# Kernel optimization log

Hardware: AMD Instinct MI355X
Metric: run time of the kernel (lower is better)

Reference implementation:

```python
import jax, jax.numpy as jnp
import numpy as np

N_TX, N_CARD, N_MERCH = 200000, 50000, 10000
E = 200000
TX_IN, EMB, H = 128, 64, 128
N_LAYERS, N_ETYPES = 2, 4  # etypes: 0 card->tx, 1 tx->card, 2 merch->tx, 3 tx->merch


def setup_inputs() -> dict:
    key = jax.random.key(0)
    ks = jax.random.split(key, 24)
    s = 0.05
    inp = {
        "tx_x": jax.random.normal(ks[0], (N_TX, TX_IN), jnp.float32),
        "card_ids": jnp.arange(N_CARD, dtype=jnp.int64),
        "merch_ids": jnp.arange(N_MERCH, dtype=jnp.int64),
        "e_card": jax.random.randint(ks[1], (E,), 0, N_CARD),
        "e_tx_c": jnp.arange(E, dtype=jnp.int64),
        "e_merch": jax.random.randint(ks[2], (E,), 0, N_MERCH),
        "e_tx_m": jnp.arange(E, dtype=jnp.int64),
        # parameters
        "card_emb": jax.random.normal(ks[3], (N_CARD, EMB), jnp.float32) * s,
        "merch_emb": jax.random.normal(ks[4], (N_MERCH, EMB), jnp.float32) * s,
        "card_proj_W": jax.random.normal(ks[5], (EMB, H), jnp.float32) * s,
        "card_proj_b": jnp.zeros((H,), jnp.float32),
        "merch_proj_W": jax.random.normal(ks[6], (EMB, H), jnp.float32) * s,
        "merch_proj_b": jnp.zeros((H,), jnp.float32),
        "tx_W": jax.random.normal(ks[7], (TX_IN, H), jnp.float32) * s,
        "tx_b": jnp.zeros((H,), jnp.float32),
        "conv_Wl": jax.random.normal(ks[8], (N_LAYERS, N_ETYPES, H, H), jnp.float32) * s,
        "conv_bl": jnp.zeros((N_LAYERS, N_ETYPES, H), jnp.float32),
        "conv_Wr": jax.random.normal(ks[9], (N_LAYERS, N_ETYPES, H, H), jnp.float32) * s,
        "h1_W": jax.random.normal(ks[10], (H, H), jnp.float32) * s,
        "h1_b": jnp.zeros((H,), jnp.float32),
        "h2_W": jax.random.normal(ks[11], (H, 1), jnp.float32) * s,
        "h2_b": jnp.zeros((1,), jnp.float32),
    }
    return inp


def _sage(x_src, x_dst, src, dst, Wl, bl, Wr, n_dst):
    # PyG SAGEConv: mean-aggregate neighbor features, then lin_l(agg)+lin_r(x_dst)
    agg = jax.ops.segment_sum(x_src[src], dst, num_segments=n_dst)
    cnt = jax.ops.segment_sum(jnp.ones((src.shape[0],), x_src.dtype), dst, num_segments=n_dst)
    mean = agg / jnp.maximum(cnt, 1.0)[:, None]
    return mean @ Wl + bl + x_dst @ Wr


def reference(tx_x, card_ids, merch_ids, e_card, e_tx_c, e_merch, e_tx_m,
              card_emb, merch_emb, card_proj_W, card_proj_b, merch_proj_W, merch_proj_b,
              tx_W, tx_b, conv_Wl, conv_bl, conv_Wr, h1_W, h1_b, h2_W, h2_b):
    # input encoders (dropout inactive at eval)
    h_tx = jax.nn.relu(tx_x @ tx_W + tx_b)
    h_card = card_emb[card_ids] @ card_proj_W + card_proj_b
    h_merch = merch_emb[merch_ids] @ merch_proj_W + merch_proj_b

    for l in range(N_LAYERS):
        Wl, bl, Wr = conv_Wl[l], conv_bl[l], conv_Wr[l]
        # HeteroConv aggr='sum' across edge types sharing a dst type
        o_tx = (_sage(h_card, h_tx, e_card, e_tx_c, Wl[0], bl[0], Wr[0], N_TX)
                + _sage(h_merch, h_tx, e_merch, e_tx_m, Wl[2], bl[2], Wr[2], N_TX))
        o_card = _sage(h_tx, h_card, e_tx_c, e_card, Wl[1], bl[1], Wr[1], N_CARD)
        o_merch = _sage(h_tx, h_merch, e_tx_m, e_merch, Wl[3], bl[3], Wr[3], N_MERCH)
        h_tx, h_card, h_merch = jax.nn.relu(o_tx), jax.nn.relu(o_card), jax.nn.relu(o_merch)

    logits = (jax.nn.relu(h_tx @ h1_W + h1_b) @ h2_W + h2_b).reshape(-1)
    return logits
```

## Files before the change

kernel.cpp:

```cpp
#include <hip/hip_runtime.h>


#define N_TX    200000
#define N_CARD  50000
#define N_MERCH 10000
#define NE      200000

typedef __attribute__((ext_vector_type(8))) short short8;
typedef __attribute__((ext_vector_type(4))) float f32x4;

__device__ inline unsigned short f2b(float f) {
    unsigned u = __builtin_bit_cast(unsigned, f);
    unsigned r = (u + 0x7fffu + ((u >> 16) & 1u)) >> 16;
    return (unsigned short)r;
}
__device__ inline float b2f(unsigned short s) {
    return __builtin_bit_cast(float, (unsigned)s << 16);
}

__global__ __launch_bounds__(256, 3) void fused2(
    const void* __restrict__ A, int a_f32,
    const unsigned short* __restrict__ W1T, const float* __restrict__ b1,
    const unsigned short* __restrict__ W2T, const float* __restrict__ b2,
    const unsigned short* __restrict__ P1, const int* __restrict__ I1,
    const unsigned short* __restrict__ P2, const int* __restrict__ I2,
    unsigned short* __restrict__ OUT0,
    const float* __restrict__ h2w, const float* __restrict__ h2b,
    void* __restrict__ OUT1, int M)
{
    __shared__ float Tf[64 * 132];
    __shared__ unsigned short Tb[64 * 136];
    const int tid  = threadIdx.x;
    const int wave = tid >> 6;
    const int lane = tid & 63;
    const int quad = lane >> 4;
    const int l15  = lane & 15;
    const int base = blockIdx.x * 64;
    const int rgrp = tid >> 4;
    const int c0   = l15 * 8;
    const bool modeA = (OUT0 != nullptr);

    int idx1[4], idx2[4];
#pragma unroll
    for (int p = 0; p < 4; ++p) {
        int r = base + p * 16 + rgrp;
        int rc = (r < M) ? r : 0;
        idx1[p] = I1 ? I1[rc] : 0;
        idx2[p] = I2 ? I2[rc] : 0;
    }

    short8 af[4];
    {
        int r = base + wave * 16 + l15;
        int rc = (r < M) ? r : 0;
        if (a_f32) {
            const float* ap = (const float*)A + (size_t)rc * 128 + quad * 8;
#pragma unroll
            for (int kk = 0; kk < 4; ++kk) {
                float4 u = *reinterpret_cast<const float4*>(ap + kk * 32);
                float4 v = *reinterpret_cast<const float4*>(ap + kk * 32 + 4);
                short8 t;
                t[0] = (short)f2b(u.x); t[1] = (short)f2b(u.y);
                t[2] = (short)f2b(u.z); t[3] = (short)f2b(u.w);
                t[4] = (short)f2b(v.x); t[5] = (short)f2b(v.y);
                t[6] = (short)f2b(v.z); t[7] = (short)f2b(v.w);
                af[kk] = t;
            }
        } else {
            const unsigned short* ap =
                (const unsigned short*)A + (size_t)rc * 128 + quad * 8;
#pragma unroll
            for (int kk = 0; kk < 4; ++kk)
                af[kk] = *reinterpret_cast<const short8*>(ap + kk * 32);
        }
    }

    f32x4 acc[8];
#pragma unroll
    for (int nt = 0; nt < 8; ++nt) acc[nt] = (f32x4){0.f, 0.f, 0.f, 0.f};
#pragma unroll
    for (int nt = 0; nt < 8; ++nt) {
        const unsigned short* bp = W1T + (nt * 16 + l15) * 128 + quad * 8;
#pragma unroll
        for (int kk = 0; kk < 4; ++kk) {
            short8 bf = *reinterpret_cast<const short8*>(bp + kk * 32);
            acc[nt] = __builtin_amdgcn_mfma_f32_16x16x32_bf16(
                af[kk], bf, acc[nt], 0, 0, 0);
        }
    }

    short8 p1v[4], p2v[4];
    if (P1) {
#pragma unroll
        for (int p = 0; p < 4; ++p)
            p1v[p] = *reinterpret_cast<const short8*>(
                P1 + (size_t)idx1[p] * 128 + c0);
    }
    if (P2) {
#pragma unroll
        for (int p = 0; p < 4; ++p)
            p2v[p] = *reinterpret_cast<const short8*>(
                P2 + (size_t)idx2[p] * 128 + c0);
    }

    const int lrow0 = wave * 16 + quad * 4;
    if (modeA) {
#pragma unroll
        for (int nt = 0; nt < 8; ++nt) {
            float bb = b1 ? b1[nt * 16 + l15] : 0.f;
#pragma unroll
            for (int reg = 0; reg < 4; ++reg)
                Tb[(lrow0 + reg) * 136 + nt * 16 + l15] =
                    f2b(fmaxf(acc[nt][reg] + bb, 0.f));
        }
    } else {
#pragma unroll
        for (int nt = 0; nt < 8; ++nt)
#pragma unroll
            for (int reg = 0; reg < 4; ++reg)
                Tf[(lrow0 + reg) * 132 + nt * 16 + l15] = acc[nt][reg];
    }
    __syncthreads();

    if (modeA) {
#pragma unroll
        for (int p = 0; p < 4; ++p) {
            const int rloc = p * 16 + rgrp;
            const int r = base + rloc;
            if (r < M) {
                short8 hv = *reinterpret_cast<const short8*>(&Tb[rloc * 136 + c0]);
                *reinterpret_cast<short8*>(OUT0 + (size_t)r * 128 + c0) = hv;
            }
        }
    } else {
        float b1r[8];
#pragma unroll
        for (int j = 0; j < 8; ++j) b1r[j] = b1 ? b1[c0 + j] : 0.f;
#pragma unroll
        for (int p = 0; p < 4; ++p) {
            const int rloc = p * 16 + rgrp;
            float4 u = *reinterpret_cast<const float4*>(&Tf[rloc * 132 + c0]);
            float4 v = *reinterpret_cast<const float4*>(&Tf[rloc * 132 + c0 + 4]);
            float o[8] = {u.x, u.y, u.z, u.w, v.x, v.y, v.z, v.w};
            short8 ov;
#pragma unroll
            for (int j = 0; j < 8; ++j) {
                float t = o[j] + b1r[j];
                if (P1) t += b2f((unsigned short)p1v[p][j]);
                if (P2) t += b2f((unsigned short)p2v[p][j]);
                ov[j] = (short)f2b(fmaxf(t, 0.f));
            }
            *reinterpret_cast<short8*>(&Tb[rloc * 136 + c0]) = ov;
        }
        __syncthreads();
    }

    short8 af2[4];
#pragma unroll
    for (int kk = 0; kk < 4; ++kk)
        af2[kk] = *reinterpret_cast<const short8*>(
            &Tb[(wave * 16 + l15) * 136 + quad * 8 + kk * 32]);

    f32x4 acc2[8];
#pragma unroll
    for (int nt = 0; nt < 8; ++nt) acc2[nt] = (f32x4){0.f, 0.f, 0.f, 0.f};
#pragma unroll
    for (int nt = 0; nt < 8; ++nt) {
        const unsigned short* bp = W2T + (nt * 16 + l15) * 128 + quad * 8;
#pragma unroll
        for (int kk = 0; kk < 4; ++kk) {
            short8 bf = *reinterpret_cast<const short8*>(bp + kk * 32);
            acc2[nt] = __builtin_amdgcn_mfma_f32_16x16x32_bf16(
                af2[kk], bf, acc2[nt], 0, 0, 0);
        }
    }

    if (!modeA) {
        float hsum[4] = {0.f, 0.f, 0.f, 0.f};
#pragma unroll
        for (int nt = 0; nt < 8; ++nt) {
            float bb = b2 ? b2[nt * 16 + l15] : 0.f;
            float w = h2w[nt * 16 + l15];
#pragma unroll
            for (int reg = 0; reg < 4; ++reg) {
                float o = fmaxf(acc2[nt][reg] + bb, 0.f);
                hsum[reg] += o * w;
            }
        }
        float* OUTf = (float*)OUT1;
#pragma unroll
        for (int reg = 0; reg < 4; ++reg) {
            float h = hsum[reg];
            h += __shfl_xor(h, 1);
            h += __shfl_xor(h, 2);
            h += __shfl_xor(h, 4);
            h += __shfl_xor(h, 8);
            int r = base + wave * 16 + quad * 4 + reg;
            if (l15 == 0 && r < M) OUTf[r] = h + h2b[0];
        }
    } else {
#pragma unroll
        for (int nt = 0; nt < 8; ++nt)
#pragma unroll
            for (int reg = 0; reg < 4; ++reg)
                Tf[(lrow0 + reg) * 132 + nt * 16 + l15] = acc2[nt][reg];
        __syncthreads();
        float b2r[8];
#pragma unroll
        for (int j = 0; j < 8; ++j) b2r[j] = b2 ? b2[c0 + j] : 0.f;
        unsigned short* OB = (unsigned short*)OUT1;
#pragma unroll
        for (int p = 0; p < 4; ++p) {
            const int rloc = p * 16 + rgrp;
            const int r = base + rloc;
            float4 u = *reinterpret_cast<const float4*>(&Tf[rloc * 132 + c0]);
            float4 v = *reinterpret_cast<const float4*>(&Tf[rloc * 132 + c0 + 4]);
            float o[8] = {u.x, u.y, u.z, u.w, v.x, v.y, v.z, v.w};
            short8 ov;
#pragma unroll
            for (int j = 0; j < 8; ++j) {
                float t = o[j] + b2r[j];
                if (P1) t += b2f((unsigned short)p1v[p][j]);
                if (P2) t += b2f((unsigned short)p2v[p][j]);
                ov[j] = (short)f2b(fmaxf(t, 0.f));
            }
            if (r < M)
                *reinterpret_cast<short8*>(OB + (size_t)r * 128 + c0) = ov;
        }
    }
}

__global__ __launch_bounds__(256, 3) void fusedE_both(
    const float* __restrict__ Ac, const unsigned short* __restrict__ W1Tc,
    const float* __restrict__ b1c, const unsigned short* __restrict__ W2Tc,
    unsigned short* __restrict__ OUT0c, unsigned short* __restrict__ OUT1c,
    int Mc, int nbc,
    const float* __restrict__ Am, const unsigned short* __restrict__ W1Tm,
    const float* __restrict__ b1m, const unsigned short* __restrict__ W2Tm,
    unsigned short* __restrict__ OUT0m, unsigned short* __restrict__ OUT1m,
    int Mm)
{
    __shared__ float Tf[64 * 132];
    __shared__ unsigned short Tb[64 * 136];
    const bool isC = (int)blockIdx.x < nbc;
    const int bx   = isC ? blockIdx.x : blockIdx.x - nbc;
    const float* A = isC ? Ac : Am;
    const unsigned short* W1T = isC ? W1Tc : W1Tm;
    const float* b1 = isC ? b1c : b1m;
    const unsigned short* W2T = isC ? W2Tc : W2Tm;
    unsigned short* OUT0 = isC ? OUT0c : OUT0m;
    unsigned short* OUT1 = isC ? OUT1c : OUT1m;
    const int M = isC ? Mc : Mm;

    const int tid  = threadIdx.x;
    const int wave = tid >> 6;
    const int lane = tid & 63;
    const int quad = lane >> 4;
    const int l15  = lane & 15;
    const int base = bx * 64;
    const int rgrp = tid >> 4;
    const int c0   = l15 * 8;

    short8 af[2];
    {
        int r = base + wave * 16 + l15;
        int rc = (r < M) ? r : 0;
        const float* ap = A + (size_t)rc * 64 + quad * 8;
#pragma unroll
        for (int kk = 0; kk < 2; ++kk) {
            float4 u = *reinterpret_cast<const float4*>(ap + kk * 32);
            float4 v = *reinterpret_cast<const float4*>(ap + kk * 32 + 4);
            short8 t;
            t[0] = (short)f2b(u.x); t[1] = (short)f2b(u.y);
            t[2] = (short)f2b(u.z); t[3] = (short)f2b(u.w);
            t[4] = (short)f2b(v.x); t[5] = (short)f2b(v.y);
            t[6] = (short)f2b(v.z); t[7] = (short)f2b(v.w);
            af[kk] = t;
        }
    }

    f32x4 acc[8];
#pragma unroll
    for (int nt = 0; nt < 8; ++nt) acc[nt] = (f32x4){0.f, 0.f, 0.f, 0.f};
#pragma unroll
    for (int nt = 0; nt < 8; ++nt) {
        const unsigned short* bp = W1T + (nt * 16 + l15) * 64 + quad * 8;
#pragma unroll
        for (int kk = 0; kk < 2; ++kk) {
            short8 bf = *reinterpret_cast<const short8*>(bp + kk * 32);
            acc[nt] = __builtin_amdgcn_mfma_f32_16x16x32_bf16(
                af[kk], bf, acc[nt], 0, 0, 0);
        }
    }

    const int lrow0 = wave * 16 + quad * 4;
#pragma unroll
    for (int nt = 0; nt < 8; ++nt) {
        float bb = b1 ? b1[nt * 16 + l15] : 0.f;
#pragma unroll
        for (int reg = 0; reg < 4; ++reg)
            Tb[(lrow0 + reg) * 136 + nt * 16 + l15] = f2b(acc[nt][reg] + bb);
    }
    __syncthreads();

#pragma unroll
    for (int p = 0; p < 4; ++p) {
        const int rloc = p * 16 + rgrp;
        const int r = base + rloc;
        if (r < M) {
            short8 hv = *reinterpret_cast<const short8*>(&Tb[rloc * 136 + c0]);
            *reinterpret_cast<short8*>(OUT0 + (size_t)r * 128 + c0) = hv;
        }
    }

    short8 af2[4];
#pragma unroll
    for (int kk = 0; kk < 4; ++kk)
        af2[kk] = *reinterpret_cast<const short8*>(
            &Tb[(wave * 16 + l15) * 136 + quad * 8 + kk * 32]);

    f32x4 acc2[8];
#pragma unroll
    for (int nt = 0; nt < 8; ++nt) acc2[nt] = (f32x4){0.f, 0.f, 0.f, 0.f};
#pragma unroll
    for (int nt = 0; nt < 8; ++nt) {
        const unsigned short* bp = W2T + (nt * 16 + l15) * 128 + quad * 8;
#pragma unroll
        for (int kk = 0; kk < 4; ++kk) {
            short8 bf = *reinterpret_cast<const short8*>(bp + kk * 32);
            acc2[nt] = __builtin_amdgcn_mfma_f32_16x16x32_bf16(
                af2[kk], bf, acc2[nt], 0, 0, 0);
        }
    }
#pragma unroll
    for (int nt = 0; nt < 8; ++nt)
#pragma unroll
        for (int reg = 0; reg < 4; ++reg)
            Tf[(lrow0 + reg) * 132 + nt * 16 + l15] = acc2[nt][reg];
    __syncthreads();
#pragma unroll
    for (int p = 0; p < 4; ++p) {
        const int rloc = p * 16 + rgrp;
        const int r = base + rloc;
        if (r >= M) continue;
        float4 u = *reinterpret_cast<const float4*>(&Tf[rloc * 132 + c0]);
        float4 v = *reinterpret_cast<const float4*>(&Tf[rloc * 132 + c0 + 4]);
        float o[8] = {u.x, u.y, u.z, u.w, v.x, v.y, v.z, v.w};
        short8 ov;
#pragma unroll
        for (int j = 0; j < 8; ++j) ov[j] = (short)f2b(o[j]);
        *reinterpret_cast<short8*>(OUT1 + (size_t)r * 128 + c0) = ov;
    }
}

__global__ __launch_bounds__(256, 3) void fusedU2_both(
    const unsigned short* __restrict__ h_src,
    const int* __restrict__ offs_c, const int* __restrict__ eidx_c,
    const unsigned short* __restrict__ A2c,
    const unsigned short* __restrict__ W1aTc, const unsigned short* __restrict__ W1bTc,
    const float* __restrict__ b1c, const unsigned short* __restrict__ W2Tc,
    unsigned short* __restrict__ OUTc, int Mc, int nbc,
    const int* __restrict__ offs_m, const int* __restrict__ eidx_m,
    const unsigned short* __restrict__ A2m,
    const unsigned short* __restrict__ W1aTm, const unsigned short* __restrict__ W1bTm,
    const float* __restrict__ b1m, const unsigned short* __restrict__ W2Tm,
    unsigned short* __restrict__ OUTm, int Mm)
{
    __shared__ float Tf[64 * 132];
    __shared__ unsigned short Tb[64 * 136];
    const bool isC = (int)blockIdx.x < nbc;
    const int bx   = isC ? blockIdx.x : blockIdx.x - nbc;
    const int* offs = isC ? offs_c : offs_m;
    const int* eidx = isC ? eidx_c : eidx_m;
    const unsigned short* A2 = isC ? A2c : A2m;
    const unsigned short* W1aT = isC ? W1aTc : W1aTm;
    const unsigned short* W1bT = isC ? W1bTc : W1bTm;
    const float* b1 = isC ? b1c : b1m;
    const unsigned short* W2T = isC ? W2Tc : W2Tm;
    unsigned short* OUT1 = isC ? OUTc : OUTm;
    const int M = isC ? Mc : Mm;

    const int tid  = threadIdx.x;
    const int wave = tid >> 6;
    const int lane = tid & 63;
    const int quad = lane >> 4;
    const int l15  = lane & 15;
    const int base = bx * 64;
    const int rgrp = tid >> 4;
    const int c0   = l15 * 8;

    for (int n = 0; n < 16; ++n) {
        const int d = base + wave * 16 + n;
        int s = 0, e = 0;
        if (d < M) { s = offs[d]; e = offs[d + 1]; }
        float a[8] = {0.f, 0.f, 0.f, 0.f, 0.f, 0.f, 0.f, 0.f};
        for (int p = s + quad; p < e; p += 4) {
            int tx = eidx[p];
            short8 v = *reinterpret_cast<const short8*>(
                h_src + (size_t)tx * 128 + l15 * 8);
#pragma unroll
            for (int j = 0; j < 8; ++j) a[j] += b2f((unsigned short)v[j]);
        }
#pragma unroll
        for (int j = 0; j < 8; ++j) {
            a[j] += __shfl_xor(a[j], 16);
            a[j] += __shfl_xor(a[j], 32);
        }
        if (quad == 0 && d < M) {
            const float inv = (e > s) ? 1.0f / (float)(e - s) : 0.f;
            short8 o;
#pragma unroll
            for (int j = 0; j < 8; ++j) o[j] = (short)f2b(a[j] * inv);
            *reinterpret_cast<short8*>(&Tb[(wave * 16 + n) * 136 + l15 * 8]) = o;
        }
    }
    __syncthreads();

    short8 afa[4], afb[4];
    {
        int r = base + wave * 16 + l15;
        int rc = (r < M) ? r : 0;
        const unsigned short* a2 = A2 + (size_t)rc * 128 + quad * 8;
#pragma unroll
        for (int kk = 0; kk < 4; ++kk) {
            afa[kk] = *reinterpret_cast<const short8*>(
                &Tb[(wave * 16 + l15) * 136 + quad * 8 + kk * 32]);
            afb[kk] = *reinterpret_cast<const short8*>(a2 + kk * 32);
        }
    }

    f32x4 acc[8];
#pragma unroll
    for (int nt = 0; nt < 8; ++nt) acc[nt] = (f32x4){0.f, 0.f, 0.f, 0.f};
#pragma unroll
    for (int nt = 0; nt < 8; ++nt) {
        const unsigned short* bpa = W1aT + (nt * 16 + l15) * 128 + quad * 8;
        const unsigned short* bpb = W1bT + (nt * 16 + l15) * 128 + quad * 8;
#pragma unroll
        for (int kk = 0; kk < 4; ++kk) {
            short8 ba = *reinterpret_cast<const short8*>(bpa + kk * 32);
            acc[nt] = __builtin_amdgcn_mfma_f32_16x16x32_bf16(
                afa[kk], ba, acc[nt], 0, 0, 0);
            short8 bb = *reinterpret_cast<const short8*>(bpb + kk * 32);
            acc[nt] = __builtin_amdgcn_mfma_f32_16x16x32_bf16(
                afb[kk], bb, acc[nt], 0, 0, 0);
        }
    }
    __syncthreads();

    const int lrow0 = wave * 16 + quad * 4;
#pragma unroll
    for (int nt = 0; nt < 8; ++nt) {
        float bv = b1 ? b1[nt * 16 + l15] : 0.f;
#pragma unroll
        for (int reg = 0; reg < 4; ++reg)
            Tb[(lrow0 + reg) * 136 + nt * 16 + l15] =
                f2b(fmaxf(acc[nt][reg] + bv, 0.f));
    }
    __syncthreads();

    short8 af2[4];
#pragma unroll
    for (int kk = 0; kk < 4; ++kk)
        af2[kk] = *reinterpret_cast<const short8*>(
            &Tb[(wave * 16 + l15) * 136 + quad * 8 + kk * 32]);

    f32x4 acc2[8];
#pragma unroll
    for (int nt = 0; nt < 8; ++nt) acc2[nt] = (f32x4){0.f, 0.f, 0.f, 0.f};
#pragma unroll
    for (int nt = 0; nt < 8; ++nt) {
        const unsigned short* bp = W2T + (nt * 16 + l15) * 128 + quad * 8;
#pragma unroll
        for (int kk = 0; kk < 4; ++kk) {
            short8 bf = *reinterpret_cast<const short8*>(bp + kk * 32);
            acc2[nt] = __builtin_amdgcn_mfma_f32_16x16x32_bf16(
                af2[kk], bf, acc2[nt], 0, 0, 0);
        }
    }
#pragma unroll
    for (int nt = 0; nt < 8; ++nt)
#pragma unroll
        for (int reg = 0; reg < 4; ++reg)
            Tf[(lrow0 + reg) * 132 + nt * 16 + l15] = acc2[nt][reg];
    __syncthreads();
#pragma unroll
    for (int p = 0; p < 4; ++p) {
        const int rloc = p * 16 + rgrp;
        const int r = base + rloc;
        if (r >= M) continue;
        float4 u = *reinterpret_cast<const float4*>(&Tf[rloc * 132 + c0]);
        float4 v = *reinterpret_cast<const float4*>(&Tf[rloc * 132 + c0 + 4]);
        float o[8] = {u.x, u.y, u.z, u.w, v.x, v.y, v.z, v.w};
        short8 ov;
#pragma unroll
        for (int j = 0; j < 8; ++j) ov[j] = (short)f2b(o[j]);
        *reinterpret_cast<short8*>(OUT1 + (size_t)r * 128 + c0) = ov;
    }
}

__global__ __launch_bounds__(256) void convert_weights(
    const float* __restrict__ tx_W, const float* __restrict__ card_proj_W,
    const float* __restrict__ merch_proj_W, const float* __restrict__ h1_W,
    const float* __restrict__ conv_Wl, const float* __restrict__ conv_Wr,
    const float* __restrict__ conv_bl,
    unsigned short* __restrict__ WT, float* __restrict__ bsum)
{
    int job = blockIdx.y;
    int K = 128;
    const float* src = nullptr;
    const float* src2 = nullptr;
    if (job == 0) src = tx_W;
    else if (job == 1) { src = card_proj_W; K = 64; }
    else if (job == 2) { src = merch_proj_W; K = 64; }
    else if (job == 3) src = h1_W;
    else {
        int l = (job - 4) / 7, e = (job - 4) % 7;
        const float* Wl = conv_Wl + (size_t)l * 4 * 16384;
        const float* Wr = conv_Wr + (size_t)l * 4 * 16384;
        switch (e) {
            case 0: src = Wl; break;
            case 1: src = Wl + 16384; break;
            case 2: src = Wl + 2 * 16384; break;
            case 3: src = Wl + 3 * 16384; break;
            case 4: src = Wr + 16384; break;
            case 5: src = Wr + 3 * 16384; break;
            default:
                src = Wr; src2 = Wr + 2 * 16384;
                if (blockIdx.x == 0 && threadIdx.x < 128) {
                    const float* bl = conv_bl + (size_t)l * 4 * 128;
                    bsum[l * 128 + threadIdx.x] =
                        bl[threadIdx.x] + bl[2 * 128 + threadIdx.x];
                }
                break;
        }
    }
    int e = blockIdx.x * 256 + threadIdx.x;
    if (e < (K << 7)) {
        int n = (K == 128) ? (e >> 7) : (e >> 6);
        int k = e & (K - 1);
        float v = src[(size_t)k * 128 + n];
        if (src2) v += src2[(size_t)k * 128 + n];
        WT[(size_t)job * 16384 + n * K + k] = f2b(v);
    }
}

__global__ __launch_bounds__(256) void hist_kernel(
    const int* __restrict__ e_card, const int* __restrict__ e_merch,
    int* __restrict__ hist_c, int* __restrict__ hist_m, int E)
{
    int i = blockIdx.x * 256 + threadIdx.x;
    if (i < E) {
        atomicAdd(&hist_c[e_card[i]], 1);
        atomicAdd(&hist_m[e_merch[i]], 1);
    }
}

__global__ __launch_bounds__(1024) void scan2_kernel(
    const int* __restrict__ hist_c, int* __restrict__ offs_c, int* __restrict__ cur_c, int nc,
    const int* __restrict__ hist_m, int* __restrict__ offs_m, int* __restrict__ cur_m, int nm)
{
    const int* hist = (blockIdx.x == 0) ? hist_c : hist_m;
    int* offs = (blockIdx.x == 0) ? offs_c : offs_m;
    int* cursor = (blockIdx.x == 0) ? cur_c : cur_m;
    int n = (blockIdx.x == 0) ? nc : nm;
    __shared__ int wsum[16];
    __shared__ int s_carry;
    const int tid = threadIdx.x, lane = tid & 63, wid = tid >> 6;
    if (tid == 0) s_carry = 0;
    __syncthreads();
    for (int base = 0; base < n; base += 8192) {
        const int i0 = base + tid * 8;
        int v[8];
        int tot = 0;
#pragma unroll
        for (int j = 0; j < 8; ++j) {
            int idx = i0 + j;
            v[j] = (idx < n) ? hist[idx] : 0;
            tot += v[j];
        }
        int x = tot;
#pragma unroll
        for (int d = 1; d < 64; d <<= 1) {
            int t = __shfl_up(x, d);
            if (lane >= d) x += t;
        }
        if (lane == 63) wsum[wid] = x;
        __syncthreads();
        if (wid == 0) {
            int y = (lane < 16) ? wsum[lane] : 0;
#pragma unroll
            for (int d = 1; d < 16; d <<= 1) {
                int t = __shfl_up(y, d);
                if (lane >= d) y += t;
            }
            if (lane < 16) wsum[lane] = y;
        }
        __syncthreads();
        int wbase = (wid > 0) ? wsum[wid - 1] : 0;
        int run = s_carry + wbase + x - tot;
#pragma unroll
        for (int j = 0; j < 8; ++j) {
            int idx = i0 + j;
            if (idx < n) { offs[idx] = run; cursor[idx] = run; }
            run += v[j];
        }
        __syncthreads();
        if (tid == 0) s_carry += wsum[15];
        __syncthreads();
    }
    if (threadIdx.x == 0) offs[n] = s_carry;
}

__global__ __launch_bounds__(256) void place_kernel(
    const int* __restrict__ e_card, const int* __restrict__ e_tx_c,
    const int* __restrict__ e_merch, const int* __restrict__ e_tx_m,
    int* __restrict__ cur_c, int* __restrict__ eidx_c,
    int* __restrict__ cur_m, int* __restrict__ eidx_m, int E)
{
    int i = blockIdx.x * 256 + threadIdx.x;
    if (i < E) {
        int pc = atomicAdd(&cur_c[e_card[i]], 1);
        eidx_c[pc] = e_tx_c[i];
        int pm = atomicAdd(&cur_m[e_merch[i]], 1);
        eidx_m[pm] = e_tx_m[i];
    }
}

extern "C" void kernel_launch(void* const* d_in, const int* in_sizes, int n_in,
                              void* d_out, int out_size, void* d_ws, size_t ws_size,
                              hipStream_t stream)
{
    const float* tx_x        = (const float*)d_in[0];
    const int*   e_card      = (const int*)d_in[3];
    const int*   e_tx_c      = (const int*)d_in[4];
    const int*   e_merch     = (const int*)d_in[5];
    const int*   e_tx_m      = (const int*)d_in[6];
    const float* card_emb    = (const float*)d_in[7];
    const float* merch_emb   = (const float*)d_in[8];
    const float* card_proj_W = (const float*)d_in[9];
    const float* card_proj_b = (const float*)d_in[10];
    const float* merch_proj_W= (const float*)d_in[11];
    const float* merch_proj_b= (const float*)d_in[12];
    const float* tx_W        = (const float*)d_in[13];
    const float* tx_b        = (const float*)d_in[14];
    const float* conv_Wl     = (const float*)d_in[15];
    const float* conv_bl     = (const float*)d_in[16];
    const float* conv_Wr     = (const float*)d_in[17];
    const float* h1_W        = (const float*)d_in[18];
    const float* h1_b        = (const float*)d_in[19];
    const float* h2_W        = (const float*)d_in[20];
    const float* h2_b        = (const float*)d_in[21];

    char* wsb = (char*)d_ws;
    auto alloc = [&](size_t bytes) {
        char* p = wsb; wsb += (bytes + 255) & ~(size_t)255; return p;
    };
    unsigned short* h_tx0    = (unsigned short*)alloc((size_t)N_TX * 128 * 2);
    unsigned short* h_tx1    = (unsigned short*)alloc((size_t)N_TX * 128 * 2);
    unsigned short* h_card0  = (unsigned short*)alloc((size_t)N_CARD * 128 * 2);
    unsigned short* h_merch0 = (unsigned short*)alloc((size_t)N_MERCH * 128 * 2);
    unsigned short* p_card   = (unsigned short*)alloc((size_t)N_CARD * 128 * 2);
    unsigned short* p_merch  = (unsigned short*)alloc((size_t)N_MERCH * 128 * 2);
    unsigned short* WT       = (unsigned short*)alloc((size_t)18 * 16384 * 2);
    float* bsum = (float*)alloc(2 * 128 * 4);
    int* hist_c = (int*)alloc((size_t)(N_CARD + N_MERCH) * 4);
    int* hist_m = hist_c + N_CARD;
    int* offs_c = (int*)alloc((size_t)(N_CARD + 1) * 4);
    int* cur_c  = (int*)alloc((size_t)N_CARD * 4);
    int* eidx_c = (int*)alloc((size_t)NE * 4);
    int* offs_m = (int*)alloc((size_t)(N_MERCH + 1) * 4);
    int* cur_m  = (int*)alloc((size_t)N_MERCH * 4);
    int* eidx_m = (int*)alloc((size_t)NE * 4);

    auto WTj = [&](int job) { return WT + (size_t)job * 16384; };

    const int nbc = (N_CARD + 63) / 64;
    const int nbm = (N_MERCH + 63) / 64;

    convert_weights<<<dim3(64, 18), dim3(256), 0, stream>>>(
        tx_W, card_proj_W, merch_proj_W, h1_W, conv_Wl, conv_Wr, conv_bl,
        WT, bsum);
    hipMemsetAsync(hist_c, 0, (size_t)(N_CARD + N_MERCH) * 4, stream);
    hist_kernel<<<dim3((NE + 255) / 256), dim3(256), 0, stream>>>(
        e_card, e_merch, hist_c, hist_m, NE);
    scan2_kernel<<<dim3(2), dim3(1024), 0, stream>>>(
        hist_c, offs_c, cur_c, N_CARD, hist_m, offs_m, cur_m, N_MERCH);
    place_kernel<<<dim3((NE + 255) / 256), dim3(256), 0, stream>>>(
        e_card, e_tx_c, e_merch, e_tx_m, cur_c, eidx_c, cur_m, eidx_m, NE);

    fusedE_both<<<dim3(nbc + nbm), dim3(256), 0, stream>>>(
        card_emb, WTj(1), card_proj_b, WTj(4), h_card0, p_card, N_CARD, nbc,
        merch_emb, WTj(2), merch_proj_b, WTj(6), h_merch0, p_merch, N_MERCH);

    fused2<<<dim3((N_TX + 63) / 64), dim3(256), 0, stream>>>(
        tx_x, 1, WTj(0), tx_b, WTj(10), bsum,
        p_card, e_card, p_merch, e_merch,
        h_tx0, nullptr, nullptr, h_tx1, N_TX);

    fusedU2_both<<<dim3(nbc + nbm), dim3(256), 0, stream>>>(
        h_tx0,
        offs_c, eidx_c, h_card0, WTj(5), WTj(8), conv_bl + 128, WTj(11),
        p_card, N_CARD, nbc,
        offs_m, eidx_m, h_merch0, WTj(7), WTj(9), conv_bl + 3 * 128, WTj(13),
        p_merch, N_MERCH);

    fused2<<<dim3((N_TX + 63) / 64), dim3(256), 0, stream>>>(
        h_tx1, 0, WTj(17), bsum + 128, WTj(3), h1_b,
        p_card, e_card, p_merch, e_merch,
        nullptr, h2_W, h2_b, d_out, N_TX);
}
```

Before: 713.9 us.

## Split neighbor mean gather into separate kernel and template fused2 on mode

Moves the CSR mean-aggregation of tx features for card and merchant nodes out of the fused update kernel into a standalone gather_mean kernel with one wave per destination node, writing bf16 means to new workspace buffers. The fused update kernel then loads those means directly as MFMA operands, dropping the in-block gather loop and two barriers. The intent is more parallelism and latency hiding for the irregular gather, which previously ran serially within each 64-row block. The cost is two extra launches and a round trip of the mean tensors through global memory. fused2 is also templated on its mode so the branch is resolved at compile time.

Result: faster. 659.6 us (-7.6%).

```diff
diff --git a/kernel.cpp b/kernel.cpp
--- a/kernel.cpp
+++ b/kernel.cpp
@@ -18,7 +18,8 @@
     return __builtin_bit_cast(float, (unsigned)s << 16);
 }
 
-__global__ __launch_bounds__(256, 3) void fused2(
+template <int MODE>
+__global__ __launch_bounds__(256, 3) void fused2k(
     const void* __restrict__ A, int a_f32,
     const unsigned short* __restrict__ W1T, const float* __restrict__ b1,
     const unsigned short* __restrict__ W2T, const float* __restrict__ b2,
@@ -28,6 +29,7 @@
     const float* __restrict__ h2w, const float* __restrict__ h2b,
     void* __restrict__ OUT1, int M)
 {
+    constexpr bool modeA = (MODE == 0);
     __shared__ float Tf[64 * 132];
     __shared__ unsigned short Tb[64 * 136];
     const int tid  = threadIdx.x;
@@ -38,7 +40,6 @@
     const int base = blockIdx.x * 64;
     const int rgrp = tid >> 4;
     const int c0   = l15 * 8;
-    const bool modeA = (OUT0 != nullptr);
 
     int idx1[4], idx2[4];
 #pragma unroll
@@ -353,15 +354,12 @@
     }
 }
 
-__global__ __launch_bounds__(256, 3) void fusedU2_both(
-    const unsigned short* __restrict__ h_src,
-    const int* __restrict__ offs_c, const int* __restrict__ eidx_c,
-    const unsigned short* __restrict__ A2c,
+__global__ __launch_bounds__(256, 3) void fusedU_both(
+    const unsigned short* __restrict__ Mc_, const unsigned short* __restrict__ A2c,
     const unsigned short* __restrict__ W1aTc, const unsigned short* __restrict__ W1bTc,
     const float* __restrict__ b1c, const unsigned short* __restrict__ W2Tc,
     unsigned short* __restrict__ OUTc, int Mc, int nbc,
-    const int* __restrict__ offs_m, const int* __restrict__ eidx_m,
-    const unsigned short* __restrict__ A2m,
+    const unsigned short* __restrict__ Mm_, const unsigned short* __restrict__ A2m,
     const unsigned short* __restrict__ W1aTm, const unsigned short* __restrict__ W1bTm,
     const float* __restrict__ b1m, const unsigned short* __restrict__ W2Tm,
     unsigned short* __restrict__ OUTm, int Mm)
@@ -370,8 +368,7 @@
     __shared__ unsigned short Tb[64 * 136];
     const bool isC = (int)blockIdx.x < nbc;
     const int bx   = isC ? blockIdx.x : blockIdx.x - nbc;
-    const int* offs = isC ? offs_c : offs_m;
-    const int* eidx = isC ? eidx_c : eidx_m;
+    const unsigned short* A1 = isC ? Mc_ : Mm_;
     const unsigned short* A2 = isC ? A2c : A2m;
     const unsigned short* W1aT = isC ? W1aTc : W1aTm;
     const unsigned short* W1bT = isC ? W1bTc : W1bTm;
@@ -389,42 +386,15 @@
     const int rgrp = tid >> 4;
     const int c0   = l15 * 8;
 
-    for (int n = 0; n < 16; ++n) {
-        const int d = base + wave * 16 + n;
-        int s = 0, e = 0;
-        if (d < M) { s = offs[d]; e = offs[d + 1]; }
-        float a[8] = {0.f, 0.f, 0.f, 0.f, 0.f, 0.f, 0.f, 0.f};
-        for (int p = s + quad; p < e; p += 4) {
-            int tx = eidx[p];
-            short8 v = *reinterpret_cast<const short8*>(
-                h_src + (size_t)tx * 128 + l15 * 8);
-#pragma unroll
-            for (int j = 0; j < 8; ++j) a[j] += b2f((unsigned short)v[j]);
-        }
-#pragma unroll
-        for (int j = 0; j < 8; ++j) {
-            a[j] += __shfl_xor(a[j], 16);
-            a[j] += __shfl_xor(a[j], 32);
-        }
-        if (quad == 0 && d < M) {
-            const float inv = (e > s) ? 1.0f / (float)(e - s) : 0.f;
-            short8 o;
-#pragma unroll
-            for (int j = 0; j < 8; ++j) o[j] = (short)f2b(a[j] * inv);
-            *reinterpret_cast<short8*>(&Tb[(wave * 16 + n) * 136 + l15 * 8]) = o;
-        }
-    }
-    __syncthreads();
-
     short8 afa[4], afb[4];
     {
         int r = base + wave * 16 + l15;
         int rc = (r < M) ? r : 0;
+        const unsigned short* a1 = A1 + (size_t)rc * 128 + quad * 8;
         const unsigned short* a2 = A2 + (size_t)rc * 128 + quad * 8;
 #pragma unroll
         for (int kk = 0; kk < 4; ++kk) {
-            afa[kk] = *reinterpret_cast<const short8*>(
-                &Tb[(wave * 16 + l15) * 136 + quad * 8 + kk * 32]);
+            afa[kk] = *reinterpret_cast<const short8*>(a1 + kk * 32);
             afb[kk] = *reinterpret_cast<const short8*>(a2 + kk * 32);
         }
     }
@@ -446,7 +416,6 @@
                 afb[kk], bb, acc[nt], 0, 0, 0);
         }
     }
-    __syncthreads();
 
     const int lrow0 = wave * 16 + quad * 4;
 #pragma unroll
@@ -627,6 +596,38 @@
     }
 }
 
+__global__ __launch_bounds__(256) void gather_mean(
+    const unsigned short* __restrict__ h_src, const int* __restrict__ offs,
+    const int* __restrict__ eidx, unsigned short* __restrict__ out_mean, int n_dst)
+{
+    const int lane = threadIdx.x & 63;
+    const int l15 = lane & 15;
+    const int quad = lane >> 4;
+    const int d = blockIdx.x * 4 + (threadIdx.x >> 6);
+    if (d >= n_dst) return;
+    const int s = offs[d], e = offs[d + 1];
+    float a[8] = {0.f, 0.f, 0.f, 0.f, 0.f, 0.f, 0.f, 0.f};
+    for (int p = s + quad; p < e; p += 4) {
+        int tx = eidx[p];
+        short8 v = *reinterpret_cast<const short8*>(
+            h_src + (size_t)tx * 128 + l15 * 8);
+#pragma unroll
+        for (int j = 0; j < 8; ++j) a[j] += b2f((unsigned short)v[j]);
+    }
+#pragma unroll
+    for (int j = 0; j < 8; ++j) {
+        a[j] += __shfl_xor(a[j], 16);
+        a[j] += __shfl_xor(a[j], 32);
+    }
+    if (quad == 0) {
+        const float inv = (e > s) ? 1.0f / (float)(e - s) : 0.f;
+        short8 o;
+#pragma unroll
+        for (int j = 0; j < 8; ++j) o[j] = (short)f2b(a[j] * inv);
+        *reinterpret_cast<short8*>(out_mean + (size_t)d * 128 + l15 * 8) = o;
+    }
+}
+
 extern "C" void kernel_launch(void* const* d_in, const int* in_sizes, int n_in,
                               void* d_out, int out_size, void* d_ws, size_t ws_size,
                               hipStream_t stream)
@@ -656,13 +657,15 @@
     auto alloc = [&](size_t bytes) {
         char* p = wsb; wsb += (bytes + 255) & ~(size_t)255; return p;
     };
-    unsigned short* h_tx0    = (unsigned short*)alloc((size_t)N_TX * 128 * 2);
-    unsigned short* h_tx1    = (unsigned short*)alloc((size_t)N_TX * 128 * 2);
-    unsigned short* h_card0  = (unsigned short*)alloc((size_t)N_CARD * 128 * 2);
-    unsigned short* h_merch0 = (unsigned short*)alloc((size_t)N_MERCH * 128 * 2);
-    unsigned short* p_card   = (unsigned short*)alloc((size_t)N_CARD * 128 * 2);
-    unsigned short* p_merch  = (unsigned short*)alloc((size_t)N_MERCH * 128 * 2);
-    unsigned short* WT       = (unsigned short*)alloc((size_t)18 * 16384 * 2);
+    unsigned short* h_tx0      = (unsigned short*)alloc((size_t)N_TX * 128 * 2);
+    unsigned short* h_tx1      = (unsigned short*)alloc((size_t)N_TX * 128 * 2);
+    unsigned short* h_card0    = (unsigned short*)alloc((size_t)N_CARD * 128 * 2);
+    unsigned short* h_merch0   = (unsigned short*)alloc((size_t)N_MERCH * 128 * 2);
+    unsigned short* p_card     = (unsigned short*)alloc((size_t)N_CARD * 128 * 2);
+    unsigned short* p_merch    = (unsigned short*)alloc((size_t)N_MERCH * 128 * 2);
+    unsigned short* mean_card  = (unsigned short*)alloc((size_t)N_CARD * 128 * 2);
+    unsigned short* mean_merch = (unsigned short*)alloc((size_t)N_MERCH * 128 * 2);
+    unsigned short* WT         = (unsigned short*)alloc((size_t)18 * 16384 * 2);
     float* bsum = (float*)alloc(2 * 128 * 4);
     int* hist_c = (int*)alloc((size_t)(N_CARD + N_MERCH) * 4);
     int* hist_m = hist_c + N_CARD;
@@ -693,19 +696,23 @@
         card_emb, WTj(1), card_proj_b, WTj(4), h_card0, p_card, N_CARD, nbc,
         merch_emb, WTj(2), merch_proj_b, WTj(6), h_merch0, p_merch, N_MERCH);
 
-    fused2<<<dim3((N_TX + 63) / 64), dim3(256), 0, stream>>>(
+    fused2k<0><<<dim3((N_TX + 63) / 64), dim3(256), 0, stream>>>(
         tx_x, 1, WTj(0), tx_b, WTj(10), bsum,
         p_card, e_card, p_merch, e_merch,
         h_tx0, nullptr, nullptr, h_tx1, N_TX);
 
-    fusedU2_both<<<dim3(nbc + nbm), dim3(256), 0, stream>>>(
-        h_tx0,
-        offs_c, eidx_c, h_card0, WTj(5), WTj(8), conv_bl + 128, WTj(11),
+    gather_mean<<<dim3((N_CARD + 3) / 4), dim3(256), 0, stream>>>(
+        h_tx0, offs_c, eidx_c, mean_card, N_CARD);
+    gather_mean<<<dim3((N_MERCH + 3) / 4), dim3(256), 0, stream>>>(
+        h_tx0, offs_m, eidx_m, mean_merch, N_MERCH);
+
+    fusedU_both<<<dim3(nbc + nbm), dim3(256), 0, stream>>>(
+        mean_card, h_card0, WTj(5), WTj(8), conv_bl + 128, WTj(11),
         p_card, N_CARD, nbc,
-        offs_m, eidx_m, h_merch0, WTj(7), WTj(9), conv_bl + 3 * 128, WTj(13),
+        mean_merch, h_merch0, WTj(7), WTj(9), conv_bl + 3 * 128, WTj(13),
         p_merch, N_MERCH);
 
-    fused2<<<dim3((N_TX + 63) / 64), dim3(256), 0, stream>>>(
+    fused2k<1><<<dim3((N_TX + 63) / 64), dim3(256), 0, stream>>>(
         h_tx1, 0, WTj(17), bsum + 128, WTj(3), h1_b,
         p_card, e_card, p_merch, e_merch,
         nullptr, h2_W, h2_b, d_out, N_TX);
```
